# Kernel tuning notes

Measured on AMD Instinct MI355X. Metric: run time of the kernel, lower is better.

Reference implementation:

```python
import jax, jax.numpy as jnp
import numpy as np

H = 1024  # hidden_size
I = 1     # input_size / output_size


def _lstm_cell(x_t, h, c, Wih, Whh, b):
    # PyTorch gate order: i, f, g, o ; Wih:[4H,I], Whh:[4H,H], b:[4H]
    gates = x_t @ Wih.T + h @ Whh.T + b          # [B, 4H]
    i, f, g, o = jnp.split(gates, 4, axis=-1)
    c_new = jax.nn.sigmoid(f) * c + jax.nn.sigmoid(i) * jnp.tanh(g)
    h_new = jax.nn.sigmoid(o) * jnp.tanh(c_new)
    return h_new, c_new


def setup_inputs() -> dict:
    key = jax.random.key(0)
    ks = jax.random.split(key, 10)
    s = 1.0 / np.sqrt(H)
    u = lambda k, shp: jax.random.uniform(k, shp, jnp.float32, -s, s)
    seq_len, batch = 512, 512
    return {
        "x": jax.random.normal(ks[0], (seq_len, batch, I), jnp.float32),
        "enc_Wih": u(ks[1], (4 * H, I)),
        "enc_Whh": u(ks[2], (4 * H, H)),
        "enc_b": u(ks[3], (4 * H,)),
        "dec_Wih": u(ks[4], (4 * H, I)),
        "dec_Whh": u(ks[5], (4 * H, H)),
        "dec_b": u(ks[6], (4 * H,)),
        "lin_W": u(ks[7], (I, H)),
        "lin_b": u(ks[8], (I,)),
        "target_len": 64,
    }


def reference(x, enc_Wih, enc_Whh, enc_b, dec_Wih, dec_Whh, dec_b, lin_W, lin_b, target_len):
    batch = x.shape[1]
    h0 = jnp.zeros((batch, H), x.dtype)
    c0 = jnp.zeros((batch, H), x.dtype)

    # Encoder: single LSTM over the full sequence; only final (h, c) is used.
    def enc_step(carry, x_t):
        h, c = carry
        h, c = _lstm_cell(x_t, h, c, enc_Wih, enc_Whh, enc_b)
        return (h, c), None

    (h, c), _ = jax.lax.scan(enc_step, (h0, c0), x)

    # Recursive decoder: feed own output back as next input.
    def dec_step(carry, _):
        h, c, y_in = carry
        h, c = _lstm_cell(y_in, h, c, dec_Wih, dec_Whh, dec_b)
        y = h @ lin_W.T + lin_b                  # [B, I]
        return (h, c, y), y

    dec_in0 = x[-1]                              # [B, I]
    _, y = jax.lax.scan(dec_step, (h, c, dec_in0), None, length=target_len)
    return y                                      # [target_len, B, I]
```

## Files before the change

kernel.cpp:

```cpp
#include <hip/hip_runtime.h>
#include <cstdint>
#include <cstddef>


#define HD    1024
#define NSTEP 576
#define TLEN  64

typedef __bf16 bf16x8 __attribute__((ext_vector_type(8)));
typedef float  f32x4  __attribute__((ext_vector_type(4)));
typedef __attribute__((address_space(1))) const unsigned int glob_u32;
typedef __attribute__((address_space(3))) unsigned int lds_u32;

__device__ __forceinline__ unsigned short f2bf(float f) {
  unsigned u = __builtin_bit_cast(unsigned, f);
  u = u + 0x7FFFu + ((u >> 16) & 1u);
  return (unsigned short)(u >> 16);
}
__device__ __forceinline__ float bf2f(unsigned short h) {
  return __builtin_bit_cast(float, (unsigned)h << 16);
}
__device__ __forceinline__ float sigm(float x) { return 1.0f / (1.0f + __expf(-x)); }
__device__ __forceinline__ float tanh_(float x) { return 1.0f - 2.0f / (1.0f + __expf(2.0f * x)); }

__global__ __launch_bounds__(256) void prep_w(const float* __restrict__ Whh,
                                              const float* __restrict__ Wih,
                                              const float* __restrict__ linW,
                                              int fold,
                                              unsigned short* __restrict__ dst) {
  int gid  = blockIdx.x * 256 + threadIdx.x;
  int rowg = gid >> 8;
  int k0   = (gid & 255) << 2;
  float4 wv = *reinterpret_cast<const float4*>(Whh + (size_t)rowg * HD + k0);
  if (fold) {
    float wi = Wih[rowg];
    float4 lw = *reinterpret_cast<const float4*>(linW + k0);
    wv.x += wi * lw.x; wv.y += wi * lw.y; wv.z += wi * lw.z; wv.w += wi * lw.w;
  }
  ushort4 hi, lo;
  hi.x = f2bf(wv.x); lo.x = f2bf(wv.x - bf2f(hi.x));
  hi.y = f2bf(wv.y); lo.y = f2bf(wv.y - bf2f(hi.y));
  hi.z = f2bf(wv.z); lo.z = f2bf(wv.z - bf2f(hi.z));
  hi.w = f2bf(wv.w); lo.w = f2bf(wv.w - bf2f(hi.w));
  int g = rowg >> 10, j = rowg & 1023;
  int tile = j >> 3, c = g * 8 + (j & 7);
  size_t base = (size_t)tile * 65536 + (size_t)c * 1024 + (size_t)(k0 ^ ((c & 7) << 3));
  *reinterpret_cast<ushort4*>(dst + base)         = hi;
  *reinterpret_cast<ushort4*>(dst + base + 32768) = lo;
}

__global__ __launch_bounds__(256) void init_out(float* __restrict__ out,
                                                const float* __restrict__ lin_b) {
  int i = blockIdx.x * 256 + threadIdx.x;
  if (i < TLEN * 512) out[i] = lin_b[0];
}

__global__ __launch_bounds__(512, 2) void lstm_persist(
    const float* __restrict__ x,
    const float* __restrict__ enc_Wih,
    const float* __restrict__ enc_b,
    const float* __restrict__ dec_Wih,
    const float* __restrict__ dec_b,
    const float* __restrict__ linW,
    const float* __restrict__ linb_p,
    const unsigned short* __restrict__ wenc,
    const unsigned short* __restrict__ wdec,
    unsigned short* __restrict__ hA,
    unsigned short* __restrict__ hB,
    float* __restrict__ p,
    unsigned* __restrict__ bar,
    float* __restrict__ out)
{
  __shared__ __align__(16) unsigned char smem[131072];
  const int tid  = threadIdx.x;
  const int lane = tid & 63;
  const int wid  = tid >> 6;
  const int l15  = lane & 15;
  const int lk   = lane >> 4;
  const int msel = (l15 >> 3) & 1;
  const int jj   = l15 & 7;

  const int bid  = blockIdx.x;
  const int rh   = (bid >> 2) & 1;
  const int tile = (bid >> 3) * 4 + (bid & 3);
  const float linb = linb_p[0];

  const int rowbase = rh * 256 + wid * 32;
  size_t aoff[2];
#pragma unroll
  for (int m = 0; m < 2; ++m)
    aoff[m] = (size_t)lk * 4096 + (size_t)(rowbase + m * 16 + l15) * 8;

  int QH[2], QL[2];
#pragma unroll
  for (int nt = 0; nt < 2; ++nt) {
    int c = nt * 16 + l15;
    int s = (c & 7) << 4;
    int q = c * 2048 + ((lk * 16) ^ s);
    QH[nt] = q;
    QL[nt] = 65536 + q;
  }

  const int erow = rowbase + msel * 16 + lk * 4;
  const size_t hobase = (size_t)tile * 4096 + (size_t)erow * 8 + jj;

  float c_reg[4] = {0.f, 0.f, 0.f, 0.f};
  float wih_r[4], b_r[4], lw_r;

#define STAGE(WB)                                                            \
  {                                                                          \
    glob_u32* gsrc = (glob_u32*)((WB) + (size_t)tile * 65536);               \
    lds_u32*  ldst = (lds_u32*)smem;                                         \
    _Pragma("unroll")                                                        \
    for (int i = 0; i < 16; ++i)                                             \
      __builtin_amdgcn_global_load_lds(gsrc + i * 2048 + tid * 4,            \
                                       ldst + i * 2048 + tid * 4, 16, 0, 0); \
  }
#define WREGS(WIH, BB)                                                       \
  {                                                                          \
    _Pragma("unroll")                                                        \
    for (int g = 0; g < 4; ++g) {                                            \
      wih_r[g] = (WIH)[g * HD + tile * 8 + jj];                              \
      b_r[g]   = (BB)[g * HD + tile * 8 + jj];                               \
    }                                                                        \
    lw_r = linW[tile * 8 + jj];                                              \
  }

  STAGE(wenc);
  WREGS(enc_Wih, enc_b);
  __syncthreads();

#pragma unroll 1
  for (int t = 0; t < NSTEP; ++t) {
    if (t == 512) {
      STAGE(wdec);
      WREGS(dec_Wih, dec_b);
      __syncthreads();
    }
    const unsigned short* hin = (t & 1) ? hB : hA;
    unsigned short* hout      = (t & 1) ? hA : hB;

    f32x4 acc[2][2] = {};
    bf16x8 Af[4][2], BH[2][2], BL[2][2];

#define LOADA(kk, st)                                                        \
  { _Pragma("unroll") for (int m = 0; m < 2; ++m)                            \
      Af[st][m] = *(const bf16x8*)(hin + (size_t)(kk) * 16384 + aoff[m]); }
#define LOADB(kk, st)                                                        \
  { _Pragma("unroll") for (int nt = 0; nt < 2; ++nt) {                       \
      BH[st][nt] = *(const bf16x8*)(smem + (QH[nt] ^ ((kk) << 6)));          \
      BL[st][nt] = *(const bf16x8*)(smem + (QL[nt] ^ ((kk) << 6))); } }

    LOADA(0, 0); LOADA(1, 1); LOADA(2, 2); LOADB(0, 0);
#pragma unroll
    for (int kk = 0; kk < 32; ++kk) {
      if (kk + 3 < 32) LOADA(kk + 3, (kk + 3) & 3);
      if (kk + 1 < 32) LOADB(kk + 1, (kk + 1) & 1);
#pragma unroll
      for (int m = 0; m < 2; ++m)
#pragma unroll
        for (int nt = 0; nt < 2; ++nt) {
          acc[m][nt] = __builtin_amdgcn_mfma_f32_16x16x32_bf16(
              Af[kk & 3][m], BH[kk & 1][nt], acc[m][nt], 0, 0, 0);
          acc[m][nt] = __builtin_amdgcn_mfma_f32_16x16x32_bf16(
              Af[kk & 3][m], BL[kk & 1][nt], acc[m][nt], 0, 0, 0);
        }
    }
#undef LOADA
#undef LOADB

    f32x4 sv0 = msel ? acc[0][0] : acc[1][0];
    f32x4 sv1 = msel ? acc[0][1] : acc[1][1];
    f32x4 w0, w1;
#pragma unroll
    for (int i = 0; i < 4; ++i) {
      w0[i] = __shfl_xor(sv0[i], 8);
      w1[i] = __shfl_xor(sv1[i], 8);
    }
    f32x4 iv = msel ? w0 : acc[0][0];
    f32x4 fv = msel ? acc[1][0] : w0;
    f32x4 gv = msel ? w1 : acc[0][1];
    f32x4 ov = msel ? acc[1][1] : w1;

    f32x4 xs;
    if (t < 512) {
      xs = *(const f32x4*)(x + (size_t)t * 512 + erow);
    } else if (t == 512) {
      f32x4 xl = *(const f32x4*)(x + (size_t)511 * 512 + erow);
      f32x4 pl = *(const f32x4*)(p + erow);
      xs = xl - pl;
    } else {
      xs = (f32x4){linb, linb, linb, linb};
    }

    float yp[4];
#pragma unroll
    for (int r = 0; r < 4; ++r) {
      float gi  = iv[r] + xs[r] * wih_r[0] + b_r[0];
      float gf  = fv[r] + xs[r] * wih_r[1] + b_r[1];
      float gg  = gv[r] + xs[r] * wih_r[2] + b_r[2];
      float go2 = ov[r] + xs[r] * wih_r[3] + b_r[3];
      float cn = sigm(gf) * c_reg[r] + sigm(gi) * tanh_(gg);
      c_reg[r] = cn;
      float hn = sigm(go2) * tanh_(cn);
      hout[hobase + (size_t)r * 8] = f2bf(hn);
      yp[r] = hn * lw_r;
    }
    if (t >= 511) {
#pragma unroll
      for (int r = 0; r < 4; ++r) {
        yp[r] += __shfl_xor(yp[r], 1);
        yp[r] += __shfl_xor(yp[r], 2);
        yp[r] += __shfl_xor(yp[r], 4);
      }
      if (jj == 0) {
        float* dst = (t == 511) ? (p + erow)
                                : (out + (size_t)(t - 512) * 512 + erow);
#pragma unroll
        for (int r = 0; r < 4; ++r) atomicAdd(dst + r, yp[r]);
      }
    }

    if (t != NSTEP - 1) {
      __syncthreads();
      if (wid == 0) {
        const unsigned tgt = (unsigned)t + 1u;
        unsigned* flags = bar + 128 + rh * 128;
        if (lane == 0) {
          __threadfence();
          __hip_atomic_store(flags + tile, tgt, __ATOMIC_RELAXED,
                             __HIP_MEMORY_SCOPE_AGENT);
        }
        if (tile == 0) {
          for (;;) {
            unsigned a = __hip_atomic_load(flags + lane, __ATOMIC_RELAXED,
                                           __HIP_MEMORY_SCOPE_AGENT);
            unsigned b = __hip_atomic_load(flags + 64 + lane, __ATOMIC_RELAXED,
                                           __HIP_MEMORY_SCOPE_AGENT);
            if (__all((a >= tgt) && (b >= tgt))) break;
            __builtin_amdgcn_s_sleep(1);
          }
          if (lane == 0)
            __hip_atomic_store(bar + rh * 32, tgt, __ATOMIC_RELAXED,
                               __HIP_MEMORY_SCOPE_AGENT);
        }
        if (lane == 0) {
          while (__hip_atomic_load(bar + rh * 32, __ATOMIC_RELAXED,
                                   __HIP_MEMORY_SCOPE_AGENT) < tgt)
            __builtin_amdgcn_s_sleep(2);
          __threadfence();
        }
      }
      __syncthreads();
    }
  }
#undef STAGE
#undef WREGS
}

extern "C" void kernel_launch(void* const* d_in, const int* in_sizes, int n_in,
                              void* d_out, int out_size, void* d_ws, size_t ws_size,
                              hipStream_t stream) {
  const float* x       = (const float*)d_in[0];
  const float* enc_Wih = (const float*)d_in[1];
  const float* enc_Whh = (const float*)d_in[2];
  const float* enc_b   = (const float*)d_in[3];
  const float* dec_Wih = (const float*)d_in[4];
  const float* dec_Whh = (const float*)d_in[5];
  const float* dec_b   = (const float*)d_in[6];
  const float* lin_W   = (const float*)d_in[7];
  const float* lin_b   = (const float*)d_in[8];
  float* out = (float*)d_out;

  uint8_t* w = (uint8_t*)d_ws;
  const size_t MB = 1u << 20;
  unsigned short* hA   = (unsigned short*)(w + 0 * MB);
  unsigned short* hB   = (unsigned short*)(w + 1 * MB);
  float*          p    = (float*)(w + 2 * MB);
  unsigned*       bar  = (unsigned*)(w + 2 * MB + 4096);
  unsigned short* wenc = (unsigned short*)(w + 4 * MB);
  unsigned short* wdec = (unsigned short*)(w + 20 * MB);

  hipMemsetAsync(hA, 0, MB, stream);
  hipMemsetAsync(p, 0, 8192, stream);
  init_out<<<128, 256, 0, stream>>>(out, lin_b);
  prep_w<<<4096, 256, 0, stream>>>(enc_Whh, enc_Wih, lin_W, 0, wenc);
  prep_w<<<4096, 256, 0, stream>>>(dec_Whh, dec_Wih, lin_W, 1, wdec);

  lstm_persist<<<256, 512, 0, stream>>>(
      x, enc_Wih, enc_b, dec_Wih, dec_b, lin_W, lin_b,
      wenc, wdec, hA, hB, p, bar, out);

  (void)in_sizes; (void)n_in; (void)out_size; (void)ws_size;
}
```

Before: 13.13 ms.

## Decentralize grid barrier and split MFMA accumulators with deeper prefetch

Replaces the two-level grid barrier, where tile 0 gathered all flags and then broadcast a release word, with a scheme in which every block's wave 0 polls all 128 per-tile flags directly. This removes one serial hop of global-memory latency from each of the 575 step barriers, at the cost of more polling traffic on the flag lines. The MFMA chain also now uses separate accumulators for the high and low bf16 weight halves, which breaks the serial dependency between paired MFMAs, and the prefetch distance is raised (A from 3 to 6 stages, B from 1 to 2) at the cost of more registers. The x-input load is moved ahead of the matmul so its latency overlaps with the MFMA work.

```diff
diff --git a/kernel.cpp b/kernel.cpp
--- a/kernel.cpp
+++ b/kernel.cpp
@@ -140,48 +140,6 @@
     const unsigned short* hin = (t & 1) ? hB : hA;
     unsigned short* hout      = (t & 1) ? hA : hB;
 
-    f32x4 acc[2][2] = {};
-    bf16x8 Af[4][2], BH[2][2], BL[2][2];
-
-#define LOADA(kk, st)                                                        \
-  { _Pragma("unroll") for (int m = 0; m < 2; ++m)                            \
-      Af[st][m] = *(const bf16x8*)(hin + (size_t)(kk) * 16384 + aoff[m]); }
-#define LOADB(kk, st)                                                        \
-  { _Pragma("unroll") for (int nt = 0; nt < 2; ++nt) {                       \
-      BH[st][nt] = *(const bf16x8*)(smem + (QH[nt] ^ ((kk) << 6)));          \
-      BL[st][nt] = *(const bf16x8*)(smem + (QL[nt] ^ ((kk) << 6))); } }
-
-    LOADA(0, 0); LOADA(1, 1); LOADA(2, 2); LOADB(0, 0);
-#pragma unroll
-    for (int kk = 0; kk < 32; ++kk) {
-      if (kk + 3 < 32) LOADA(kk + 3, (kk + 3) & 3);
-      if (kk + 1 < 32) LOADB(kk + 1, (kk + 1) & 1);
-#pragma unroll
-      for (int m = 0; m < 2; ++m)
-#pragma unroll
-        for (int nt = 0; nt < 2; ++nt) {
-          acc[m][nt] = __builtin_amdgcn_mfma_f32_16x16x32_bf16(
-              Af[kk & 3][m], BH[kk & 1][nt], acc[m][nt], 0, 0, 0);
-          acc[m][nt] = __builtin_amdgcn_mfma_f32_16x16x32_bf16(
-              Af[kk & 3][m], BL[kk & 1][nt], acc[m][nt], 0, 0, 0);
-        }
-    }
-#undef LOADA
-#undef LOADB
-
-    f32x4 sv0 = msel ? acc[0][0] : acc[1][0];
-    f32x4 sv1 = msel ? acc[0][1] : acc[1][1];
-    f32x4 w0, w1;
-#pragma unroll
-    for (int i = 0; i < 4; ++i) {
-      w0[i] = __shfl_xor(sv0[i], 8);
-      w1[i] = __shfl_xor(sv1[i], 8);
-    }
-    f32x4 iv = msel ? w0 : acc[0][0];
-    f32x4 fv = msel ? acc[1][0] : w0;
-    f32x4 gv = msel ? w1 : acc[0][1];
-    f32x4 ov = msel ? acc[1][1] : w1;
-
     f32x4 xs;
     if (t < 512) {
       xs = *(const f32x4*)(x + (size_t)t * 512 + erow);
@@ -192,6 +150,57 @@
     } else {
       xs = (f32x4){linb, linb, linb, linb};
     }
+
+    f32x4 accH[2][2] = {};
+    f32x4 accL[2][2] = {};
+    bf16x8 Af[8][2], BH[4][2], BL[4][2];
+
+#define LOADA(kk, st)                                                        \
+  { _Pragma("unroll") for (int m = 0; m < 2; ++m)                            \
+      Af[st][m] = *(const bf16x8*)(hin + (size_t)(kk) * 16384 + aoff[m]); }
+#define LOADB(kk, st)                                                        \
+  { _Pragma("unroll") for (int nt = 0; nt < 2; ++nt) {                       \
+      BH[st][nt] = *(const bf16x8*)(smem + (QH[nt] ^ ((kk) << 6)));          \
+      BL[st][nt] = *(const bf16x8*)(smem + (QL[nt] ^ ((kk) << 6))); } }
+
+    LOADA(0, 0); LOADA(1, 1); LOADA(2, 2); LOADA(3, 3); LOADA(4, 4); LOADA(5, 5);
+    LOADB(0, 0); LOADB(1, 1);
+#pragma unroll
+    for (int kk = 0; kk < 32; ++kk) {
+      if (kk + 6 < 32) LOADA(kk + 6, (kk + 6) & 7);
+      if (kk + 2 < 32) LOADB(kk + 2, (kk + 2) & 3);
+#pragma unroll
+      for (int m = 0; m < 2; ++m)
+#pragma unroll
+        for (int nt = 0; nt < 2; ++nt) {
+          accH[m][nt] = __builtin_amdgcn_mfma_f32_16x16x32_bf16(
+              Af[kk & 7][m], BH[kk & 3][nt], accH[m][nt], 0, 0, 0);
+          accL[m][nt] = __builtin_amdgcn_mfma_f32_16x16x32_bf16(
+              Af[kk & 7][m], BL[kk & 3][nt], accL[m][nt], 0, 0, 0);
+        }
+    }
+#undef LOADA
+#undef LOADB
+
+    f32x4 acc[2][2];
+#pragma unroll
+    for (int m = 0; m < 2; ++m)
+#pragma unroll
+      for (int nt = 0; nt < 2; ++nt)
+        acc[m][nt] = accH[m][nt] + accL[m][nt];
+
+    f32x4 sv0 = msel ? acc[0][0] : acc[1][0];
+    f32x4 sv1 = msel ? acc[0][1] : acc[1][1];
+    f32x4 w0, w1;
+#pragma unroll
+    for (int i = 0; i < 4; ++i) {
+      w0[i] = __shfl_xor(sv0[i], 8);
+      w1[i] = __shfl_xor(sv1[i], 8);
+    }
+    f32x4 iv = msel ? w0 : acc[0][0];
+    f32x4 fv = msel ? acc[1][0] : w0;
+    f32x4 gv = msel ? w1 : acc[0][1];
+    f32x4 ov = msel ? acc[1][1] : w1;
 
     float yp[4];
 #pragma unroll
@@ -231,25 +240,15 @@
           __hip_atomic_store(flags + tile, tgt, __ATOMIC_RELAXED,
                              __HIP_MEMORY_SCOPE_AGENT);
         }
-        if (tile == 0) {
-          for (;;) {
-            unsigned a = __hip_atomic_load(flags + lane, __ATOMIC_RELAXED,
-                                           __HIP_MEMORY_SCOPE_AGENT);
-            unsigned b = __hip_atomic_load(flags + 64 + lane, __ATOMIC_RELAXED,
-                                           __HIP_MEMORY_SCOPE_AGENT);
-            if (__all((a >= tgt) && (b >= tgt))) break;
-            __builtin_amdgcn_s_sleep(1);
-          }
-          if (lane == 0)
-            __hip_atomic_store(bar + rh * 32, tgt, __ATOMIC_RELAXED,
-                               __HIP_MEMORY_SCOPE_AGENT);
+        for (;;) {
+          unsigned a = __hip_atomic_load(flags + lane, __ATOMIC_RELAXED,
+                                         __HIP_MEMORY_SCOPE_AGENT);
+          unsigned b = __hip_atomic_load(flags + 64 + lane, __ATOMIC_RELAXED,
+                                         __HIP_MEMORY_SCOPE_AGENT);
+          if (__all((a >= tgt) && (b >= tgt))) break;
+          __builtin_amdgcn_s_sleep(1);
         }
-        if (lane == 0) {
-          while (__hip_atomic_load(bar + rh * 32, __ATOMIC_RELAXED,
-                                   __HIP_MEMORY_SCOPE_AGENT) < tgt)
-            __builtin_amdgcn_s_sleep(2);
-          __threadfence();
-        }
+        __threadfence();
       }
       __syncthreads();
     }
```

Measured after the change: 14.97 ms. +14.0%, slower.
